# Kernel optimization log

Measured on AMD Instinct MI355X. Metric: run time of the kernel, lower is better.

The kernel has to match this reference:

```python
import jax, jax.numpy as jnp
import numpy as np

B, C, N = 8, 256, 4096
K = C // 4  # projection dim for F and G (feat_dim // 4)


def setup_inputs() -> dict:
    key = jax.random.key(0)
    k1, k2, k3, k4, k5, k6 = jax.random.split(key, 6)
    inp = {
        "input": jax.random.normal(k1, (B, C, N), dtype=jnp.float32),
        "nms_feat": jax.random.normal(k2, (B, C, N), dtype=jnp.float32),
        "WF": jax.random.normal(k3, (K, C), dtype=jnp.float32) * (1.0 / np.sqrt(C)),
        "WG": jax.random.normal(k4, (K, C), dtype=jnp.float32) * (1.0 / np.sqrt(C)),
        "WH": jax.random.normal(k5, (C, C), dtype=jnp.float32) * (1.0 / np.sqrt(C)),
        "gamma": jax.random.normal(k6, (1,), dtype=jnp.float32),
    }
    return inp


def reference(input, nms_feat, WF, WG, WH, gamma):
    feat = nms_feat  # [B, C, N]; module uses nms_feat when provided
    b, c, n = feat.shape
    # 1x1 conv projections == channel matmuls; outputs laid out as [B, N, d]
    f = jnp.einsum('kc,bcn->bnk', WF, feat)   # [B, N, K]
    g = jnp.einsum('kc,bcn->bnk', WG, feat)   # [B, N, K]
    h = jnp.einsum('dc,bcn->bnd', WH, feat)   # [B, N, C]
    # attention scores (no scaling in original module)
    s = jnp.einsum('bnk,bmk->bnm', g, f)      # [B, N, N]
    beta = jax.nn.softmax(s, axis=-1)
    o = jnp.einsum('bnm,bmd->bnd', beta, h)   # [B, N, C]
    # NOTE: the original does a raw reshape [B,N,C] -> [B,C,N] (not a transpose);
    # we reproduce that exactly.
    o = o.reshape(b, c, n)
    return gamma * o + input
```

## Files before the change

kernel.cpp:

```cpp
#include <hip/hip_runtime.h>
#include <hip/hip_bf16.h>

#define BB 8
#define CC 256
#define NN 4096
#define KP 64
#define LOG2E 1.44269504088896f

typedef _Float16 f16x8 __attribute__((ext_vector_type(8)));
typedef _Float16 f16x4 __attribute__((ext_vector_type(4)));
typedef float    f32x4 __attribute__((ext_vector_type(4)));

#define MFMA16(a, b, c) __builtin_amdgcn_mfma_f32_16x16x32_f16((a), (b), (c), 0, 0, 0)

__device__ __forceinline__ float fast_exp2(float x) {
#if __has_builtin(__builtin_amdgcn_exp2f)
    return __builtin_amdgcn_exp2f(x);
#else
    return __expf(x * 0.69314718055994531f);
#endif
}

template<int CTRL>
__device__ __forceinline__ float dpp_ror_f(float x) {
    return __int_as_float(__builtin_amdgcn_update_dpp(
        0, __float_as_int(x), CTRL, 0xF, 0xF, true));
}
__device__ __forceinline__ float max16(float x) {
    x = fmaxf(x, dpp_ror_f<0x128>(x));
    x = fmaxf(x, dpp_ror_f<0x124>(x));
    x = fmaxf(x, dpp_ror_f<0x122>(x));
    x = fmaxf(x, dpp_ror_f<0x121>(x));
    return x;
}
__device__ __forceinline__ float sum16(float x) {
    x += dpp_ror_f<0x128>(x);
    x += dpp_ror_f<0x124>(x);
    x += dpp_ror_f<0x122>(x);
    x += dpp_ror_f<0x121>(x);
    return x;
}

__global__ __launch_bounds__(256) void wconv_kernel(
    const float* __restrict__ WF, const float* __restrict__ WG,
    const float* __restrict__ WH, _Float16* __restrict__ W16)
{
    int gid = blockIdx.x * 256 + threadIdx.x;
    int i4  = gid * 4;
    const float* src;
    if (i4 < 64 * CC)        src = WF + i4;
    else if (i4 < 128 * CC)  src = WG + (i4 - 64 * CC);
    else                     src = WH + (i4 - 128 * CC);
    float4 v = *(const float4*)src;
    f16x4 o = { (_Float16)v.x, (_Float16)v.y, (_Float16)v.z, (_Float16)v.w };
    *(f16x4*)(W16 + i4) = o;
}

__global__ __launch_bounds__(256, 3) void proj16_kernel(
    const float* __restrict__ feat, const _Float16* __restrict__ W16,
    _Float16* __restrict__ fb, _Float16* __restrict__ gb,
    _Float16* __restrict__ hT)
{
    __shared__ __align__(16) _Float16 ft[64][264];
    const int b = blockIdx.y, n0 = blockIdx.x * 64, t = threadIdx.x;

    #pragma unroll
    for (int i = 0; i < 16; i++) {
        int v = t + i * 256, c = v >> 4, nq = v & 15;
        float4 x = *(const float4*)(feat + ((size_t)b * CC + c) * NN + n0 + nq * 4);
        ft[nq * 4 + 0][c] = (_Float16)x.x;
        ft[nq * 4 + 1][c] = (_Float16)x.y;
        ft[nq * 4 + 2][c] = (_Float16)x.z;
        ft[nq * 4 + 3][c] = (_Float16)x.w;
    }
    __syncthreads();

    const int w = t >> 6, lane = t & 63, quad = lane >> 4, ln = lane & 15;
    const int rowbase = w * 96;

    f32x4 acc[6][4] = {};
    #pragma unroll
    for (int ks = 0; ks < 8; ks++) {
        const int c0 = ks * 32;
        f16x8 bfr[4];
        #pragma unroll
        for (int tf = 0; tf < 4; tf++)
            bfr[tf] = *(const f16x8*)&ft[tf * 16 + ln][c0 + quad * 8];
        #pragma unroll
        for (int af = 0; af < 6; af++) {
            f16x8 a = *(const f16x8*)(W16 + (size_t)(rowbase + af * 16 + ln) * CC + c0 + quad * 8);
            #pragma unroll
            for (int tf = 0; tf < 4; tf++)
                acc[af][tf] = MFMA16(a, bfr[tf], acc[af][tf]);
        }
    }

    #pragma unroll
    for (int af = 0; af < 6; af++) {
        const int orow0 = rowbase + af * 16 + quad * 4;
        if (orow0 < 64) {
            #pragma unroll
            for (int tf = 0; tf < 4; tf++) {
                const int tok = n0 + tf * 16 + ln;
                f16x4 pk = { (_Float16)acc[af][tf][0], (_Float16)acc[af][tf][1],
                             (_Float16)acc[af][tf][2], (_Float16)acc[af][tf][3] };
                *(f16x4*)(fb + ((size_t)b * NN + tok) * KP + orow0) = pk;
            }
        } else if (orow0 < 128) {
            #pragma unroll
            for (int tf = 0; tf < 4; tf++) {
                const int tok = n0 + tf * 16 + ln;
                f16x4 pk = { (_Float16)(acc[af][tf][0] * LOG2E),
                             (_Float16)(acc[af][tf][1] * LOG2E),
                             (_Float16)(acc[af][tf][2] * LOG2E),
                             (_Float16)(acc[af][tf][3] * LOG2E) };
                *(f16x4*)(gb + ((size_t)b * NN + tok) * KP + (orow0 - 64)) = pk;
            }
        } else {
            #pragma unroll
            for (int r = 0; r < 4; r++) {
                const int d = orow0 - 128 + r;
                f16x4 pk = { (_Float16)acc[af][0][r], (_Float16)acc[af][1][r],
                             (_Float16)acc[af][2][r], (_Float16)acc[af][3][r] };
                *(f16x4*)(hT + ((size_t)b * CC + d) * NN + n0 + ln * 4) = pk;
            }
        }
    }
}

__global__ __launch_bounds__(256, 2) void attn16_kernel(
    const _Float16* __restrict__ fb, const _Float16* __restrict__ gb,
    const _Float16* __restrict__ hT, const float* __restrict__ inp,
    const float* __restrict__ gamma, float* __restrict__ out)
{
    __shared__ __align__(16) _Float16 g_s[64][72];
    __shared__ __align__(16) _Float16 f_s[64][72];
    __shared__ __align__(16) _Float16 p_s[64][72];
    __shared__ float alpha_s[64];
    __shared__ float l_s[64];

    const int b = blockIdx.x, q0 = blockIdx.y * 64, t = threadIdx.x;
    const int w = t >> 6, lane = t & 63, quad = lane >> 4, ln = lane & 15;
    const int row = t >> 2, kq = t & 3;
    const int dbase = w * 64;

    {
        const _Float16* src = gb + ((size_t)b * NN + q0 + row) * KP + kq * 16;
        *(f16x8*)&g_s[row][kq * 16]     = *(const f16x8*)(src);
        *(f16x8*)&g_s[row][kq * 16 + 8] = *(const f16x8*)(src + 8);
    }
    f16x8 fr0, fr1;
    {
        const _Float16* src = fb + ((size_t)b * NN + row) * KP + kq * 16;
        fr0 = *(const f16x8*)(src);
        fr1 = *(const f16x8*)(src + 8);
    }
    __syncthreads();

    f16x8 ag[2];
    ag[0] = *(const f16x8*)&g_s[w * 16 + ln][quad * 8];
    ag[1] = *(const f16x8*)&g_s[w * 16 + ln][32 + quad * 8];

    float m_run[4] = {-1e30f, -1e30f, -1e30f, -1e30f};
    float l_run[4] = {0.f, 0.f, 0.f, 0.f};
    f32x4 acc[4][4] = {};
    f16x8 hv[2][4];

    #pragma unroll 1
    for (int mt = 0; mt < NN / 64; mt++) {
        const int m0 = mt * 64;

        *(f16x8*)&f_s[row][kq * 16]     = fr0;
        *(f16x8*)&f_s[row][kq * 16 + 8] = fr1;
        __syncthreads();

        {
            const int m0n = ((mt + 1) & 63) * 64;
            const _Float16* srcf = fb + ((size_t)b * NN + m0n + row) * KP + kq * 16;
            fr0 = *(const f16x8*)(srcf);
            fr1 = *(const f16x8*)(srcf + 8);
            #pragma unroll
            for (int ks = 0; ks < 2; ks++)
                #pragma unroll
                for (int df = 0; df < 4; df++)
                    hv[ks][df] = *(const f16x8*)(hT +
                        ((size_t)b * CC + dbase + df * 16 + ln) * NN + m0 + ks * 32 + quad * 8);
        }

        f32x4 S[4] = {};
        #pragma unroll
        for (int ks = 0; ks < 2; ks++) {
            #pragma unroll
            for (int mf = 0; mf < 4; mf++) {
                f16x8 bf = *(const f16x8*)&f_s[mf * 16 + ln][ks * 32 + quad * 8];
                S[mf] = MFMA16(ag[ks], bf, S[mf]);
            }
        }

        #pragma unroll
        for (int r = 0; r < 4; r++) {
            float mx = fmaxf(fmaxf(S[0][r], S[1][r]), fmaxf(S[2][r], S[3][r]));
            mx = max16(mx);
            float mnew = fmaxf(m_run[r], mx);
            float al   = fast_exp2(m_run[r] - mnew);
            float p0 = fast_exp2(S[0][r] - mnew);
            float p1 = fast_exp2(S[1][r] - mnew);
            float p2 = fast_exp2(S[2][r] - mnew);
            float p3 = fast_exp2(S[3][r] - mnew);
            float sum = sum16((p0 + p1) + (p2 + p3));
            l_run[r] = l_run[r] * al + sum;
            m_run[r] = mnew;
            const int qrow = w * 16 + quad * 4 + r;
            if (ln == 0) alpha_s[qrow] = al;
            f16x4 pk = { (_Float16)p0, (_Float16)p1, (_Float16)p2, (_Float16)p3 };
            *(f16x4*)&p_s[qrow][ln * 4] = pk;
        }
        __syncthreads();

        float al_[4][4];
        bool need = false;
        #pragma unroll
        for (int qf = 0; qf < 4; qf++)
            #pragma unroll
            for (int r = 0; r < 4; r++) {
                al_[qf][r] = alpha_s[qf * 16 + quad * 4 + r];
                need |= (al_[qf][r] != 1.0f);
            }
        if (__ballot(need)) {
            #pragma unroll
            for (int qf = 0; qf < 4; qf++)
                #pragma unroll
                for (int df = 0; df < 4; df++)
                    #pragma unroll
                    for (int r = 0; r < 4; r++)
                        acc[qf][df][r] *= al_[qf][r];
        }

        #pragma unroll
        for (int ks = 0; ks < 2; ks++) {
            #pragma unroll
            for (int qf = 0; qf < 4; qf++) {
                f16x8 ap = *(const f16x8*)&p_s[qf * 16 + ln][ks * 32 + quad * 8];
                #pragma unroll
                for (int df = 0; df < 4; df++)
                    acc[qf][df] = MFMA16(ap, hv[ks][df], acc[qf][df]);
            }
        }
    }

    if (ln == 0) {
        #pragma unroll
        for (int r = 0; r < 4; r++) l_s[w * 16 + quad * 4 + r] = l_run[r];
    }
    __syncthreads();

    const float gam = gamma[0];
    #pragma unroll
    for (int qf = 0; qf < 4; qf++) {
        #pragma unroll
        for (int r = 0; r < 4; r++) {
            const int q = qf * 16 + quad * 4 + r;
            const float linv = 1.0f / l_s[q];
            #pragma unroll
            for (int df = 0; df < 4; df++) {
                const int d = dbase + df * 16 + ln;
                size_t idx = ((size_t)b * NN + q0 + q) * CC + d;
                out[idx] = fmaf(gam, acc[qf][df][r] * linv, inp[idx]);
            }
        }
    }
}

extern "C" void kernel_launch(void* const* d_in, const int* in_sizes, int n_in,
                              void* d_out, int out_size, void* d_ws, size_t ws_size,
                              hipStream_t stream) {
    const float* input = (const float*)d_in[0];
    const float* nms   = (const float*)d_in[1];
    const float* WF    = (const float*)d_in[2];
    const float* WG    = (const float*)d_in[3];
    const float* WH    = (const float*)d_in[4];
    const float* gamma = (const float*)d_in[5];
    float* out = (float*)d_out;

    char* ws = (char*)d_ws;
    _Float16* W16  = (_Float16*)ws;
    _Float16* fb16 = (_Float16*)(ws + 196608);
    _Float16* gb16 = (_Float16*)(ws + 196608 + 4194304);
    _Float16* hT16 = (_Float16*)(ws + 196608 + 2 * 4194304);

    wconv_kernel<<<96, 256, 0, stream>>>(WF, WG, WH, W16);
    proj16_kernel<<<dim3(NN / 64, BB), 256, 0, stream>>>(nms, W16, fb16, gb16, hT16);
    attn16_kernel<<<dim3(BB, NN / 64), 256, 0, stream>>>(fb16, gb16, hT16, input, gamma, out);
}
```

Baseline: 257.5 us.

## Double attention key tile to 128 and load G fragments directly from global

The attention loop now processes 128 keys per iteration instead of 64. This halves the number of barriers and online-softmax rescale steps per query block. The G fragments are read straight from global memory into registers, which removes the g_s shared buffer and the initial sync. The f_s and p_s shared tiles are resized with new padding, and alpha is read back as float4. The projection kernel's feat load is split into batched loads followed by stores to raise memory-level parallelism. In exchange, the per-iteration H loads double and register pressure grows (hv[4][4], S[8]), which may reduce occupancy.

```diff
diff --git a/kernel.cpp b/kernel.cpp
--- a/kernel.cpp
+++ b/kernel.cpp
@@ -65,13 +65,23 @@
     const int b = blockIdx.y, n0 = blockIdx.x * 64, t = threadIdx.x;
 
     #pragma unroll
-    for (int i = 0; i < 16; i++) {
-        int v = t + i * 256, c = v >> 4, nq = v & 15;
-        float4 x = *(const float4*)(feat + ((size_t)b * CC + c) * NN + n0 + nq * 4);
-        ft[nq * 4 + 0][c] = (_Float16)x.x;
-        ft[nq * 4 + 1][c] = (_Float16)x.y;
-        ft[nq * 4 + 2][c] = (_Float16)x.z;
-        ft[nq * 4 + 3][c] = (_Float16)x.w;
+    for (int half = 0; half < 2; half++) {
+        float4 tmp[8];
+        #pragma unroll
+        for (int i = 0; i < 8; i++) {
+            int v = t + (half * 8 + i) * 256;
+            int c = v >> 4, nq = v & 15;
+            tmp[i] = *(const float4*)(feat + ((size_t)b * CC + c) * NN + n0 + nq * 4);
+        }
+        #pragma unroll
+        for (int i = 0; i < 8; i++) {
+            int v = t + (half * 8 + i) * 256;
+            int c = v >> 4, nq = v & 15;
+            ft[nq * 4 + 0][c] = (_Float16)tmp[i].x;
+            ft[nq * 4 + 1][c] = (_Float16)tmp[i].y;
+            ft[nq * 4 + 2][c] = (_Float16)tmp[i].z;
+            ft[nq * 4 + 3][c] = (_Float16)tmp[i].w;
+        }
     }
     __syncthreads();
 
@@ -133,111 +143,118 @@
     const _Float16* __restrict__ hT, const float* __restrict__ inp,
     const float* __restrict__ gamma, float* __restrict__ out)
 {
-    __shared__ __align__(16) _Float16 g_s[64][72];
-    __shared__ __align__(16) _Float16 f_s[64][72];
-    __shared__ __align__(16) _Float16 p_s[64][72];
+    __shared__ __align__(16) _Float16 f_s[128][66];
+    __shared__ __align__(16) _Float16 p_s[64][130];
     __shared__ float alpha_s[64];
     __shared__ float l_s[64];
 
     const int b = blockIdx.x, q0 = blockIdx.y * 64, t = threadIdx.x;
     const int w = t >> 6, lane = t & 63, quad = lane >> 4, ln = lane & 15;
-    const int row = t >> 2, kq = t & 3;
     const int dbase = w * 64;
-
+    const int srow = t & 127, scol = (t >> 7) * 32;
+
+    const _Float16* gsrc = gb + ((size_t)b * NN + q0 + w * 16 + ln) * KP + quad * 8;
+    f16x8 ag0 = *(const f16x8*)(gsrc);
+    f16x8 ag1 = *(const f16x8*)(gsrc + 32);
+
+    f16x8 fr[4];
     {
-        const _Float16* src = gb + ((size_t)b * NN + q0 + row) * KP + kq * 16;
-        *(f16x8*)&g_s[row][kq * 16]     = *(const f16x8*)(src);
-        *(f16x8*)&g_s[row][kq * 16 + 8] = *(const f16x8*)(src + 8);
-    }
-    f16x8 fr0, fr1;
-    {
-        const _Float16* src = fb + ((size_t)b * NN + row) * KP + kq * 16;
-        fr0 = *(const f16x8*)(src);
-        fr1 = *(const f16x8*)(src + 8);
-    }
-    __syncthreads();
-
-    f16x8 ag[2];
-    ag[0] = *(const f16x8*)&g_s[w * 16 + ln][quad * 8];
-    ag[1] = *(const f16x8*)&g_s[w * 16 + ln][32 + quad * 8];
+        const _Float16* src = fb + ((size_t)b * NN + srow) * KP + scol;
+        fr[0] = *(const f16x8*)(src);
+        fr[1] = *(const f16x8*)(src + 8);
+        fr[2] = *(const f16x8*)(src + 16);
+        fr[3] = *(const f16x8*)(src + 24);
+    }
 
     float m_run[4] = {-1e30f, -1e30f, -1e30f, -1e30f};
     float l_run[4] = {0.f, 0.f, 0.f, 0.f};
     f32x4 acc[4][4] = {};
-    f16x8 hv[2][4];
 
     #pragma unroll 1
-    for (int mt = 0; mt < NN / 64; mt++) {
-        const int m0 = mt * 64;
-
-        *(f16x8*)&f_s[row][kq * 16]     = fr0;
-        *(f16x8*)&f_s[row][kq * 16 + 8] = fr1;
+    for (int mt = 0; mt < NN / 128; mt++) {
+        const int m0 = mt * 128;
+
+        *(f16x8*)&f_s[srow][scol]      = fr[0];
+        *(f16x8*)&f_s[srow][scol + 8]  = fr[1];
+        *(f16x8*)&f_s[srow][scol + 16] = fr[2];
+        *(f16x8*)&f_s[srow][scol + 24] = fr[3];
         __syncthreads();
 
         {
-            const int m0n = ((mt + 1) & 63) * 64;
-            const _Float16* srcf = fb + ((size_t)b * NN + m0n + row) * KP + kq * 16;
-            fr0 = *(const f16x8*)(srcf);
-            fr1 = *(const f16x8*)(srcf + 8);
-            #pragma unroll
-            for (int ks = 0; ks < 2; ks++)
-                #pragma unroll
-                for (int df = 0; df < 4; df++)
-                    hv[ks][df] = *(const f16x8*)(hT +
-                        ((size_t)b * CC + dbase + df * 16 + ln) * NN + m0 + ks * 32 + quad * 8);
-        }
-
-        f32x4 S[4] = {};
-        #pragma unroll
-        for (int ks = 0; ks < 2; ks++) {
-            #pragma unroll
-            for (int mf = 0; mf < 4; mf++) {
-                f16x8 bf = *(const f16x8*)&f_s[mf * 16 + ln][ks * 32 + quad * 8];
-                S[mf] = MFMA16(ag[ks], bf, S[mf]);
-            }
+            const int m0n = ((mt + 1) & 31) * 128;
+            const _Float16* src = fb + ((size_t)b * NN + m0n + srow) * KP + scol;
+            fr[0] = *(const f16x8*)(src);
+            fr[1] = *(const f16x8*)(src + 8);
+            fr[2] = *(const f16x8*)(src + 16);
+            fr[3] = *(const f16x8*)(src + 24);
+        }
+        f16x8 hv[4][4];
+        #pragma unroll
+        for (int ks = 0; ks < 4; ks++)
+            #pragma unroll
+            for (int df = 0; df < 4; df++)
+                hv[ks][df] = *(const f16x8*)(hT +
+                    ((size_t)b * CC + dbase + df * 16 + ln) * NN + m0 + ks * 32 + quad * 8);
+
+        f32x4 S[8];
+        #pragma unroll
+        for (int mf = 0; mf < 8; mf++) {
+            f16x8 bf0 = *(const f16x8*)&f_s[mf * 16 + ln][quad * 8];
+            f16x8 bf1 = *(const f16x8*)&f_s[mf * 16 + ln][32 + quad * 8];
+            f32x4 s = {};
+            s = MFMA16(ag0, bf0, s);
+            s = MFMA16(ag1, bf1, s);
+            S[mf] = s;
         }
 
         #pragma unroll
         for (int r = 0; r < 4; r++) {
-            float mx = fmaxf(fmaxf(S[0][r], S[1][r]), fmaxf(S[2][r], S[3][r]));
+            float mx = fmaxf(fmaxf(fmaxf(S[0][r], S[1][r]), fmaxf(S[2][r], S[3][r])),
+                             fmaxf(fmaxf(S[4][r], S[5][r]), fmaxf(S[6][r], S[7][r])));
             mx = max16(mx);
             float mnew = fmaxf(m_run[r], mx);
             float al   = fast_exp2(m_run[r] - mnew);
-            float p0 = fast_exp2(S[0][r] - mnew);
-            float p1 = fast_exp2(S[1][r] - mnew);
-            float p2 = fast_exp2(S[2][r] - mnew);
-            float p3 = fast_exp2(S[3][r] - mnew);
-            float sum = sum16((p0 + p1) + (p2 + p3));
+            float p[8];
+            float sum = 0.f;
+            #pragma unroll
+            for (int mf = 0; mf < 8; mf++) {
+                p[mf] = fast_exp2(S[mf][r] - mnew);
+                sum += p[mf];
+            }
+            sum = sum16(sum);
             l_run[r] = l_run[r] * al + sum;
             m_run[r] = mnew;
             const int qrow = w * 16 + quad * 4 + r;
             if (ln == 0) alpha_s[qrow] = al;
-            f16x4 pk = { (_Float16)p0, (_Float16)p1, (_Float16)p2, (_Float16)p3 };
-            *(f16x4*)&p_s[qrow][ln * 4] = pk;
+            f16x4 pkLo = { (_Float16)p[0], (_Float16)p[1], (_Float16)p[2], (_Float16)p[3] };
+            f16x4 pkHi = { (_Float16)p[4], (_Float16)p[5], (_Float16)p[6], (_Float16)p[7] };
+            *(f16x4*)&p_s[qrow][ln * 4]      = pkLo;
+            *(f16x4*)&p_s[qrow][64 + ln * 4] = pkHi;
         }
         __syncthreads();
 
-        float al_[4][4];
+        float4 alv[4];
         bool need = false;
         #pragma unroll
-        for (int qf = 0; qf < 4; qf++)
-            #pragma unroll
-            for (int r = 0; r < 4; r++) {
-                al_[qf][r] = alpha_s[qf * 16 + quad * 4 + r];
-                need |= (al_[qf][r] != 1.0f);
-            }
+        for (int qf = 0; qf < 4; qf++) {
+            alv[qf] = *(const float4*)&alpha_s[qf * 16 + quad * 4];
+            need |= (alv[qf].x != 1.0f) | (alv[qf].y != 1.0f) |
+                    (alv[qf].z != 1.0f) | (alv[qf].w != 1.0f);
+        }
         if (__ballot(need)) {
             #pragma unroll
             for (int qf = 0; qf < 4; qf++)
                 #pragma unroll
-                for (int df = 0; df < 4; df++)
-                    #pragma unroll
-                    for (int r = 0; r < 4; r++)
-                        acc[qf][df][r] *= al_[qf][r];
-        }
-
-        #pragma unroll
-        for (int ks = 0; ks < 2; ks++) {
+                for (int df = 0; df < 4; df++) {
+                    acc[qf][df][0] *= alv[qf].x;
+                    acc[qf][df][1] *= alv[qf].y;
+                    acc[qf][df][2] *= alv[qf].z;
+                    acc[qf][df][3] *= alv[qf].w;
+                }
+        }
+
+        #pragma unroll
+        for (int ks = 0; ks < 4; ks++) {
             #pragma unroll
             for (int qf = 0; qf < 4; qf++) {
                 f16x8 ap = *(const f16x8*)&p_s[qf * 16 + ln][ks * 32 + quad * 8];
```

New measurement: 309.2 us. 20.1% more time.
